# Performance work log

Hardware: AMD Instinct MI355X
Metric: run time of the kernel (lower is better)

The kernel has to match this reference:

```python
import jax, jax.numpy as jnp
import numpy as np

EPS = 1e-6

def _grad_magnitude(x):
    # x: [B, 1, D, H, W]. Valid 3x3x3 conv with shift-subtract kernels:
    # kernel_w differences along D, kernel_d along H, kernel_h along W.
    g_w = x[:, :, 2:, 1:-1, 1:-1] - x[:, :, :-2, 1:-1, 1:-1]
    g_d = x[:, :, 1:-1, 2:, 1:-1] - x[:, :, 1:-1, :-2, 1:-1]
    g_h = x[:, :, 1:-1, 1:-1, 2:] - x[:, :, 1:-1, 1:-1, :-2]
    mag = jnp.sqrt(g_w * g_w + g_d * g_d + g_h * g_h + EPS)
    # replicate-pad back to original spatial size
    return jnp.pad(mag, ((0, 0), (0, 0), (1, 1), (1, 1), (1, 1)), mode='edge')

def setup_inputs() -> dict:
    key = jax.random.key(0)
    k1, k2 = jax.random.split(key)
    shape = (1, 1, 256, 256, 256)
    x1 = jax.random.normal(k1, shape, dtype=jnp.float32)
    x2 = jax.random.normal(k2, shape, dtype=jnp.float32)
    return {"x1": x1, "x2": x2}

def reference(x1, x2):
    g1 = _grad_magnitude(x1)
    g2 = _grad_magnitude(x2)
    return jnp.mean(jnp.abs(g1 - g2))
```

## Files before the change

kernel.cpp:

```cpp
#include <hip/hip_runtime.h>


__global__ __launch_bounds__(256) void grad_loss_kernel(const float4* __restrict__ x1,
                                                        const float4* __restrict__ x2,
                                                        double* __restrict__ acc) {
    const int tid   = threadIdx.x;
    const int lane  = tid & 63;
    const int hslot = tid >> 6;
    const int htile = blockIdx.x & 63;
    const int dchk  = blockIdx.x >> 6;

    const int h  = 1 + htile * 4 + hslot;
    const int d0 = 1 + dchk * 4;

    float ww0, ww1, ww2, ww3;
    {
        const int wbase = 4 * lane;
        ww0 = (wbase + 0 == 0)   ? 0.0f : ((wbase + 0 == 1)   ? 2.0f : 1.0f);
        ww1 = (wbase + 1 == 1)   ? 2.0f : 1.0f;
        ww2 = (wbase + 2 == 254) ? 2.0f : 1.0f;
        ww3 = (wbase + 3 == 255) ? 0.0f : ((wbase + 3 == 254) ? 2.0f : 1.0f);
    }

    float val = 0.0f;

    if (h <= 254) {
        const float whf = (h == 1 || h == 254) ? 2.0f : 1.0f;
        const int rowbase = h * 64 + lane;

        float4 a1 = x1[(d0 - 1) * 16384 + rowbase];
        float4 b1 = x1[d0 * 16384 + rowbase];
        float4 a2 = x2[(d0 - 1) * 16384 + rowbase];
        float4 b2 = x2[d0 * 16384 + rowbase];

        const int dend = (d0 + 4 <= 255) ? (d0 + 4) : 255;
        for (int d = d0; d < dend; ++d) {
            const int base = d * 16384 + rowbase;
            float4 c1 = x1[base + 16384];
            float4 u1 = x1[base - 64];
            float4 v1 = x1[base + 64];
            float4 c2 = x2[base + 16384];
            float4 u2 = x2[base - 64];
            float4 v2 = x2[base + 64];

            float l1 = __shfl_up(b1.w, 1, 64);
            float r1 = __shfl_down(b1.x, 1, 64);
            float l2 = __shfl_up(b2.w, 1, 64);
            float r2 = __shfl_down(b2.x, 1, 64);

            float gw, gd, gh, m10, m11, m12, m13, m20, m21, m22, m23;

            gw = c1.x - a1.x; gd = v1.x - u1.x; gh = b1.y - l1;
            m10 = sqrtf(gw * gw + gd * gd + gh * gh + 1e-6f);
            gw = c1.y - a1.y; gd = v1.y - u1.y; gh = b1.z - b1.x;
            m11 = sqrtf(gw * gw + gd * gd + gh * gh + 1e-6f);
            gw = c1.z - a1.z; gd = v1.z - u1.z; gh = b1.w - b1.y;
            m12 = sqrtf(gw * gw + gd * gd + gh * gh + 1e-6f);
            gw = c1.w - a1.w; gd = v1.w - u1.w; gh = r1 - b1.z;
            m13 = sqrtf(gw * gw + gd * gd + gh * gh + 1e-6f);

            gw = c2.x - a2.x; gd = v2.x - u2.x; gh = b2.y - l2;
            m20 = sqrtf(gw * gw + gd * gd + gh * gh + 1e-6f);
            gw = c2.y - a2.y; gd = v2.y - u2.y; gh = b2.z - b2.x;
            m21 = sqrtf(gw * gw + gd * gd + gh * gh + 1e-6f);
            gw = c2.z - a2.z; gd = v2.z - u2.z; gh = b2.w - b2.y;
            m22 = sqrtf(gw * gw + gd * gd + gh * gh + 1e-6f);
            gw = c2.w - a2.w; gd = v2.w - u2.w; gh = r2 - b2.z;
            m23 = sqrtf(gw * gw + gd * gd + gh * gh + 1e-6f);

            float inner = ww0 * fabsf(m10 - m20)
                        + ww1 * fabsf(m11 - m21)
                        + ww2 * fabsf(m12 - m22)
                        + ww3 * fabsf(m13 - m23);

            const float wdf = (d == 1 || d == 254) ? 2.0f : 1.0f;
            val += wdf * whf * inner;

            a1 = b1; b1 = c1;
            a2 = b2; b2 = c2;
        }
    }

    for (int off = 32; off > 0; off >>= 1)
        val += __shfl_down(val, off, 64);

    __shared__ float smem[4];
    const int lid = tid & 63;
    const int wid = tid >> 6;
    if (lid == 0) smem[wid] = val;
    __syncthreads();

    if (wid == 0) {
        float s = (lid < 4) ? smem[lid] : 0.0f;
        s += __shfl_down(s, 2, 64);
        s += __shfl_down(s, 1, 64);
        if (lid == 0)
            atomicAdd(&acc[blockIdx.x & 255], (double)s);
    }
}

__global__ void finalize_kernel(const double* __restrict__ acc, float* __restrict__ out) {
    double v = acc[threadIdx.x];
    for (int off = 32; off > 0; off >>= 1)
        v += __shfl_down(v, off, 64);

    __shared__ double smem[4];
    const int lid = threadIdx.x & 63;
    const int wid = threadIdx.x >> 6;
    if (lid == 0) smem[wid] = v;
    __syncthreads();

    if (threadIdx.x == 0) {
        double s = smem[0] + smem[1] + smem[2] + smem[3];
        out[0] = (float)(s / 16777216.0);
    }
}

extern "C" void kernel_launch(void* const* d_in, const int* in_sizes, int n_in,
                              void* d_out, int out_size, void* d_ws, size_t ws_size,
                              hipStream_t stream) {
    const float4* x1 = (const float4*)d_in[0];
    const float4* x2 = (const float4*)d_in[1];
    float* out = (float*)d_out;
    double* acc = (double*)d_ws;

    hipMemsetAsync(d_ws, 0, 256 * sizeof(double), stream);
    grad_loss_kernel<<<64 * 64, 256, 0, stream>>>(x1, x2, acc);
    finalize_kernel<<<1, 256, 0, stream>>>(acc, out);
}
```

Measured before the change: 159.0 us.

## Software-pipeline depth loop with prefetch, larger depth chunk, native sqrt

Each block now processes 8 depth slices instead of 4, halving the grid, and the loop is fully unrolled with the next slice's center, neighbor-row and W-halo loads issued before the current slice's math. The W-direction halo values are loaded directly from memory instead of exchanged with wavefront shuffles. sqrtf is replaced with the hardware sqrt builtin. This aims to hide global load latency and trim ALU work, at the cost of more registers and fewer blocks for occupancy.

```diff
diff --git a/kernel.cpp b/kernel.cpp
--- a/kernel.cpp
+++ b/kernel.cpp
@@ -1,9 +1,14 @@
 #include <hip/hip_runtime.h>
 
 
-__global__ __launch_bounds__(256) void grad_loss_kernel(const float4* __restrict__ x1,
-                                                        const float4* __restrict__ x2,
+#define CHUNK 8
+
+__global__ __launch_bounds__(256) void grad_loss_kernel(const float* __restrict__ xf1,
+                                                        const float* __restrict__ xf2,
                                                         double* __restrict__ acc) {
+    const float4* __restrict__ x1 = (const float4*)xf1;
+    const float4* __restrict__ x2 = (const float4*)xf2;
+
     const int tid   = threadIdx.x;
     const int lane  = tid & 63;
     const int hslot = tid >> 6;
@@ -11,73 +16,89 @@
     const int dchk  = blockIdx.x >> 6;
 
     const int h  = 1 + htile * 4 + hslot;
-    const int d0 = 1 + dchk * 4;
+    const int d0 = 1 + dchk * CHUNK;
 
-    float ww0, ww1, ww2, ww3;
-    {
-        const int wbase = 4 * lane;
-        ww0 = (wbase + 0 == 0)   ? 0.0f : ((wbase + 0 == 1)   ? 2.0f : 1.0f);
-        ww1 = (wbase + 1 == 1)   ? 2.0f : 1.0f;
-        ww2 = (wbase + 2 == 254) ? 2.0f : 1.0f;
-        ww3 = (wbase + 3 == 255) ? 0.0f : ((wbase + 3 == 254) ? 2.0f : 1.0f);
-    }
+    const int wbase = 4 * lane;
+    const float ww0 = (wbase + 0 == 0)   ? 0.0f : 1.0f;
+    const float ww1 = (wbase + 1 == 1)   ? 2.0f : 1.0f;
+    const float ww2 = (wbase + 2 == 254) ? 2.0f : 1.0f;
+    const float ww3 = (wbase + 3 == 255) ? 0.0f : 1.0f;
 
     float val = 0.0f;
 
     if (h <= 254) {
         const float whf = (h == 1 || h == 254) ? 2.0f : 1.0f;
         const int rowbase = h * 64 + lane;
+        const int frow    = h * 256 + wbase;
 
         float4 a1 = x1[(d0 - 1) * 16384 + rowbase];
         float4 b1 = x1[d0 * 16384 + rowbase];
         float4 a2 = x2[(d0 - 1) * 16384 + rowbase];
         float4 b2 = x2[d0 * 16384 + rowbase];
+        float  l1 = xf1[d0 * 65536 + frow - 1];
+        float  r1 = xf1[d0 * 65536 + frow + 4];
+        float  l2 = xf2[d0 * 65536 + frow - 1];
+        float  r2 = xf2[d0 * 65536 + frow + 4];
+        float4 c1 = x1[(d0 + 1) * 16384 + rowbase];
+        float4 u1 = x1[d0 * 16384 + rowbase - 64];
+        float4 v1 = x1[d0 * 16384 + rowbase + 64];
+        float4 c2 = x2[(d0 + 1) * 16384 + rowbase];
+        float4 u2 = x2[d0 * 16384 + rowbase - 64];
+        float4 v2 = x2[d0 * 16384 + rowbase + 64];
 
-        const int dend = (d0 + 4 <= 255) ? (d0 + 4) : 255;
-        for (int d = d0; d < dend; ++d) {
-            const int base = d * 16384 + rowbase;
-            float4 c1 = x1[base + 16384];
-            float4 u1 = x1[base - 64];
-            float4 v1 = x1[base + 64];
-            float4 c2 = x2[base + 16384];
-            float4 u2 = x2[base - 64];
-            float4 v2 = x2[base + 64];
+        #pragma unroll
+        for (int i = 0; i < CHUNK; ++i) {
+            const int d = d0 + i;
 
-            float l1 = __shfl_up(b1.w, 1, 64);
-            float r1 = __shfl_down(b1.x, 1, 64);
-            float l2 = __shfl_up(b2.w, 1, 64);
-            float r2 = __shfl_down(b2.x, 1, 64);
+            float4 nc1, nu1, nv1, nc2, nu2, nv2;
+            float  nl1, nr1, nl2, nr2;
+            if (i < CHUNK - 1) {
+                const int dn = (d + 1 <= 254) ? (d + 1) : 254;
+                const int nb = dn * 16384 + rowbase;
+                const int nf = dn * 65536 + frow;
+                nc1 = x1[nb + 16384];
+                nu1 = x1[nb - 64];
+                nv1 = x1[nb + 64];
+                nl1 = xf1[nf - 1];
+                nr1 = xf1[nf + 4];
+                nc2 = x2[nb + 16384];
+                nu2 = x2[nb - 64];
+                nv2 = x2[nb + 64];
+                nl2 = xf2[nf - 1];
+                nr2 = xf2[nf + 4];
+            }
 
-            float gw, gd, gh, m10, m11, m12, m13, m20, m21, m22, m23;
-
+            float gw, gd, gh;
             gw = c1.x - a1.x; gd = v1.x - u1.x; gh = b1.y - l1;
-            m10 = sqrtf(gw * gw + gd * gd + gh * gh + 1e-6f);
+            float m10 = __builtin_amdgcn_sqrtf(gw * gw + gd * gd + gh * gh + 1e-6f);
             gw = c1.y - a1.y; gd = v1.y - u1.y; gh = b1.z - b1.x;
-            m11 = sqrtf(gw * gw + gd * gd + gh * gh + 1e-6f);
+            float m11 = __builtin_amdgcn_sqrtf(gw * gw + gd * gd + gh * gh + 1e-6f);
             gw = c1.z - a1.z; gd = v1.z - u1.z; gh = b1.w - b1.y;
-            m12 = sqrtf(gw * gw + gd * gd + gh * gh + 1e-6f);
+            float m12 = __builtin_amdgcn_sqrtf(gw * gw + gd * gd + gh * gh + 1e-6f);
             gw = c1.w - a1.w; gd = v1.w - u1.w; gh = r1 - b1.z;
-            m13 = sqrtf(gw * gw + gd * gd + gh * gh + 1e-6f);
+            float m13 = __builtin_amdgcn_sqrtf(gw * gw + gd * gd + gh * gh + 1e-6f);
 
             gw = c2.x - a2.x; gd = v2.x - u2.x; gh = b2.y - l2;
-            m20 = sqrtf(gw * gw + gd * gd + gh * gh + 1e-6f);
+            float m20 = __builtin_amdgcn_sqrtf(gw * gw + gd * gd + gh * gh + 1e-6f);
             gw = c2.y - a2.y; gd = v2.y - u2.y; gh = b2.z - b2.x;
-            m21 = sqrtf(gw * gw + gd * gd + gh * gh + 1e-6f);
+            float m21 = __builtin_amdgcn_sqrtf(gw * gw + gd * gd + gh * gh + 1e-6f);
             gw = c2.z - a2.z; gd = v2.z - u2.z; gh = b2.w - b2.y;
-            m22 = sqrtf(gw * gw + gd * gd + gh * gh + 1e-6f);
+            float m22 = __builtin_amdgcn_sqrtf(gw * gw + gd * gd + gh * gh + 1e-6f);
             gw = c2.w - a2.w; gd = v2.w - u2.w; gh = r2 - b2.z;
-            m23 = sqrtf(gw * gw + gd * gd + gh * gh + 1e-6f);
+            float m23 = __builtin_amdgcn_sqrtf(gw * gw + gd * gd + gh * gh + 1e-6f);
 
             float inner = ww0 * fabsf(m10 - m20)
                         + ww1 * fabsf(m11 - m21)
                         + ww2 * fabsf(m12 - m22)
                         + ww3 * fabsf(m13 - m23);
 
-            const float wdf = (d == 1 || d == 254) ? 2.0f : 1.0f;
+            const float wdf = (d > 254) ? 0.0f : ((d == 1 || d == 254) ? 2.0f : 1.0f);
             val += wdf * whf * inner;
 
-            a1 = b1; b1 = c1;
-            a2 = b2; b2 = c2;
+            if (i < CHUNK - 1) {
+                a1 = b1; b1 = c1; c1 = nc1; u1 = nu1; v1 = nv1; l1 = nl1; r1 = nr1;
+                a2 = b2; b2 = c2; c2 = nc2; u2 = nu2; v2 = nv2; l2 = nl2; r2 = nr2;
+            }
         }
     }
 
@@ -119,12 +140,12 @@
 extern "C" void kernel_launch(void* const* d_in, const int* in_sizes, int n_in,
                               void* d_out, int out_size, void* d_ws, size_t ws_size,
                               hipStream_t stream) {
-    const float4* x1 = (const float4*)d_in[0];
-    const float4* x2 = (const float4*)d_in[1];
+    const float* x1 = (const float*)d_in[0];
+    const float* x2 = (const float*)d_in[1];
     float* out = (float*)d_out;
     double* acc = (double*)d_ws;
 
     hipMemsetAsync(d_ws, 0, 256 * sizeof(double), stream);
-    grad_loss_kernel<<<64 * 64, 256, 0, stream>>>(x1, x2, acc);
+    grad_loss_kernel<<<64 * 32, 256, 0, stream>>>(x1, x2, acc);
     finalize_kernel<<<1, 256, 0, stream>>>(acc, out);
 }
```

Result: no change. 157.5 us (-0.9%).
